# Performance work log

Measured on AMD Instinct MI355X. Metric: run time of the kernel, lower is better.

The kernel has to match this reference:

```python
import jax, jax.numpy as jnp
import numpy as np

B, S, D_MODEL, H = 2, 2048, 1024, 16
DK = D_MODEL // H
THETA = 10000.0


def setup_inputs() -> dict:
    key = jax.random.key(0)
    ks = jax.random.split(key, 5)
    scale = 0.02  # keep logits in a numerically sane range
    return {
        "x": jax.random.normal(ks[0], (B, S, D_MODEL), jnp.float32),
        "Q_weight": jax.random.normal(ks[1], (D_MODEL, D_MODEL), jnp.float32) * scale,
        "K_weight": jax.random.normal(ks[2], (D_MODEL, D_MODEL), jnp.float32) * scale,
        "V_weight": jax.random.normal(ks[3], (D_MODEL, D_MODEL), jnp.float32) * scale,
        "O_weight": jax.random.normal(ks[4], (D_MODEL, D_MODEL), jnp.float32) * scale,
        "token_positions": jnp.arange(S, dtype=jnp.int32),
    }


def _rope(x, token_positions, theta, d_k):
    # x: [..., seq, d_k]; rotate interleaved even/odd pairs
    inv_freq = 1.0 / theta ** (jnp.arange(0, d_k, 2, dtype=jnp.float32) / d_k)
    ang = token_positions.astype(jnp.float32)[:, None] * inv_freq  # [S, d_k/2]
    cos, sin = jnp.cos(ang), jnp.sin(ang)
    x0, x1 = x[..., 0::2], x[..., 1::2]
    y0 = x0 * cos - x1 * sin
    y1 = x0 * sin + x1 * cos
    return jnp.stack([y0, y1], axis=-1).reshape(x.shape)


def _mhsa(x, Qw, Kw, Vw, Ow, token_positions):
    b, s, d = x.shape
    qw = Qw.reshape(H, DK, d)
    kw = Kw.reshape(H, DK, d)
    vw = Vw.reshape(H, DK, d)
    q = jnp.einsum('hki,bsi->bhsk', qw, x)
    k = jnp.einsum('hki,bsi->bhsk', kw, x)
    v = jnp.einsum('hvi,bsi->bhsv', vw, x)
    q = _rope(q, token_positions, THETA, DK)
    k = _rope(k, token_positions, THETA, DK)
    scores = jnp.einsum('bhnd,bhmd->bhnm', q, k) / jnp.sqrt(jnp.float32(DK))
    causal = jnp.tril(jnp.ones((s, s), dtype=bool))
    scores = jnp.where(causal, scores, -jnp.inf)
    attn = jax.nn.softmax(scores, axis=-1)
    o = jnp.einsum('bhnm,bhmv->bhnv', attn, v)  # [B,H,S,DV]
    o = jnp.transpose(o, (0, 2, 1, 3)).reshape(b, s, H * DK)
    return jnp.einsum('dv,bsv->bsd', Ow, o)


def reference(x, Q_weight, K_weight, V_weight, O_weight, token_positions):
    return _mhsa(x, Q_weight, K_weight, V_weight, O_weight, token_positions)
```

## Files before the change

kernel.cpp:

```cpp
#include <hip/hip_runtime.h>

#define NB 2
#define NS 2048
#define NDM 1024
#define NH 16
#define NDK 64

typedef unsigned int u32;
typedef u32 u32x4 __attribute__((ext_vector_type(4)));
typedef float f32x4 __attribute__((ext_vector_type(4)));
typedef float f32x2 __attribute__((ext_vector_type(2)));
typedef __bf16 bf16x8 __attribute__((ext_vector_type(8)));
typedef __bf16 bf16x4 __attribute__((ext_vector_type(4)));
typedef __bf16 bf16x2 __attribute__((ext_vector_type(2)));

#define QSCALE 0.18033688011112042f
#define EXP2F(x) __builtin_amdgcn_exp2f(x)

__device__ __forceinline__ void gload_lds16(const __bf16* g, __bf16* l) {
    __builtin_amdgcn_global_load_lds(
        (const __attribute__((address_space(1))) unsigned int*)(g),
        (__attribute__((address_space(3))) unsigned int*)(l), 16, 0, 0);
}

__global__ __launch_bounds__(256) void cvt_all(const float* __restrict__ x,
                                               const float* __restrict__ qw,
                                               const float* __restrict__ kw,
                                               const float* __restrict__ vw,
                                               const float* __restrict__ ow,
                                               __bf16* __restrict__ xb,
                                               __bf16* __restrict__ wqkv,
                                               __bf16* __restrict__ owb) {
    const int i = blockIdx.x * 256 + threadIdx.x;
    const float* src;
    __bf16* dst;
    if (i < 1048576) {
        src = x + (size_t)i * 4;
        dst = xb + (size_t)i * 4;
    } else {
        const int j = i - 1048576;
        const int seg = j >> 18;
        const int off = j & 0x3FFFF;
        src = ((seg == 0) ? qw : (seg == 1) ? kw : (seg == 2) ? vw : ow) + (size_t)off * 4;
        dst = ((seg == 3) ? owb : wqkv + (size_t)seg * 1048576) + (size_t)off * 4;
    }
    f32x4 v = *(const f32x4*)src;
    bf16x4 o;
    o[0] = (__bf16)v[0]; o[1] = (__bf16)v[1]; o[2] = (__bf16)v[2]; o[3] = (__bf16)v[3];
    *(bf16x4*)dst = o;
}

__global__ __launch_bounds__(256) void rope_table(const int* __restrict__ tp,
                                                  float* __restrict__ tbl) {
    const int i = blockIdx.x * 256 + threadIdx.x;
    if (i >= NS * 32) return;
    const int s = i >> 5, jj = i & 31;
    const float pos = (float)tp[s];
    const float inv = exp2f(-0.41524101186092f * (float)jj);
    const float ang = pos * inv;
    float sn, cs;
    sincosf(ang, &sn, &cs);
    f32x2 o; o[0] = cs; o[1] = sn;
    *(f32x2*)&tbl[(size_t)i * 2] = o;
}

__global__ __launch_bounds__(512, 2) void gemm256(const __bf16* __restrict__ A,
                                                  const __bf16* __restrict__ Bt,
                                                  __bf16* __restrict__ C,
                                                  int K, int lda, int ldb, int ldc, int nbx) {
    __shared__ __bf16 As[2][256 * 64];
    __shared__ __bf16 Bs[2][256 * 64];
    const int tid = threadIdx.x;
    const int lane = tid & 63, w = tid >> 6;
    const int wm = w >> 2, wn = w & 3;
    const int l15 = lane & 15, lg = lane >> 4;
    int bid = blockIdx.x;
    const int cpx = gridDim.x >> 3;
    bid = (bid & 7) * cpx + (bid >> 3);
    const int m0 = (bid / nbx) * 256, n0 = (bid % nbx) * 256;
    const int srow = w * 8 + (lane >> 3);
    const int csw = ((lane & 7) ^ (srow & 7)) * 8;

    f32x4 acc[8][4];
    const f32x4 z = {0.f, 0.f, 0.f, 0.f};
#pragma unroll
    for (int i = 0; i < 8; ++i)
#pragma unroll
        for (int jx = 0; jx < 4; ++jx) acc[i][jx] = z;

    auto stage_pass = [&](int buf, int k0, int ps) {
        const int r = ps * 64 + srow;
        gload_lds16(&A[(size_t)(m0 + r) * lda + k0 + csw], &As[buf][(ps * 64 + w * 8) * 64]);
        gload_lds16(&Bt[(size_t)(n0 + r) * ldb + k0 + csw], &Bs[buf][(ps * 64 + w * 8) * 64]);
    };

#pragma unroll
    for (int ps = 0; ps < 4; ++ps) stage_pass(0, 0, ps);
    int cur = 0;
    for (int k0 = 0; k0 < K; k0 += 64) {
        const bool hasnext = (k0 + 64 < K);
        asm volatile("s_waitcnt vmcnt(0)" ::: "memory");
        __builtin_amdgcn_s_barrier();
        __builtin_amdgcn_sched_barrier(0);
        bf16x8 bfr[4][2];
#pragma unroll
        for (int ph = 0; ph < 4; ++ph) {
            if (ph == 0) {
#pragma unroll
                for (int n = 0; n < 4; ++n)
#pragma unroll
                    for (int kc = 0; kc < 2; ++kc) {
                        const int rb = wn * 64 + n * 16 + l15;
                        bfr[n][kc] = *(const bf16x8*)&Bs[cur][rb * 64 + ((kc * 32 + lg * 8) ^ ((rb & 7) << 3))];
                    }
            }
            bf16x8 a0[2], a1[2];
#pragma unroll
            for (int kc = 0; kc < 2; ++kc) {
                const int ra0 = wm * 128 + (2 * ph) * 16 + l15;
                const int ra1 = wm * 128 + (2 * ph + 1) * 16 + l15;
                a0[kc] = *(const bf16x8*)&As[cur][ra0 * 64 + ((kc * 32 + lg * 8) ^ ((ra0 & 7) << 3))];
                a1[kc] = *(const bf16x8*)&As[cur][ra1 * 64 + ((kc * 32 + lg * 8) ^ ((ra1 & 7) << 3))];
            }
            if (hasnext) stage_pass(cur ^ 1, k0 + 64, ph);
            __builtin_amdgcn_s_barrier();
            asm volatile("s_waitcnt lgkmcnt(0)" ::: "memory");
            __builtin_amdgcn_sched_barrier(0);
            __builtin_amdgcn_s_setprio(1);
#pragma unroll
            for (int n = 0; n < 4; ++n)
#pragma unroll
                for (int kc = 0; kc < 2; ++kc) {
                    acc[2 * ph][n]     = __builtin_amdgcn_mfma_f32_16x16x32_bf16(a0[kc], bfr[n][kc], acc[2 * ph][n], 0, 0, 0);
                    acc[2 * ph + 1][n] = __builtin_amdgcn_mfma_f32_16x16x32_bf16(a1[kc], bfr[n][kc], acc[2 * ph + 1][n], 0, 0, 0);
                }
            __builtin_amdgcn_s_setprio(0);
            __builtin_amdgcn_s_barrier();
            __builtin_amdgcn_sched_barrier(0);
        }
        cur ^= 1;
    }
#pragma unroll
    for (int mr = 0; mr < 8; ++mr)
#pragma unroll
        for (int n = 0; n < 4; ++n)
#pragma unroll
            for (int j = 0; j < 4; ++j) {
                const int row = m0 + wm * 128 + mr * 16 + lg * 4 + j;
                const int col = n0 + wn * 64 + n * 16 + l15;
                C[(size_t)row * ldc + col] = (__bf16)acc[mr][n][j];
            }
}

template <typename TOUT>
__global__ __launch_bounds__(256) void gemm_bt128(const __bf16* __restrict__ A,
                                                  const __bf16* __restrict__ Bt,
                                                  TOUT* __restrict__ C,
                                                  int K, int lda, int ldb, int ldc) {
    __shared__ __bf16 As[2][128 * 64];
    __shared__ __bf16 Bs[2][128 * 64];
    const int tid = threadIdx.x;
    const int lane = tid & 63, w = tid >> 6;
    const int wr = w >> 1, wc = w & 1;
    const int l15 = lane & 15, lg = lane >> 4;
    const int m0 = blockIdx.y * 128, n0 = blockIdx.x * 128;
    const int crow = lane >> 3;
    const int csw = ((lane & 7) ^ crow) * 8;

    f32x4 acc[4][4];
    const f32x4 z = {0.f, 0.f, 0.f, 0.f};
#pragma unroll
    for (int i = 0; i < 4; ++i)
#pragma unroll
        for (int jx = 0; jx < 4; ++jx) acc[i][jx] = z;

    auto stage = [&](int buf, int k0) {
#pragma unroll
        for (int ch = 0; ch < 4; ++ch) {
            const int cid = w * 4 + ch;
            const int ra = cid * 8 + crow;
            gload_lds16(&A[(size_t)(m0 + ra) * lda + k0 + csw], &As[buf][cid * 512]);
            gload_lds16(&Bt[(size_t)(n0 + ra) * ldb + k0 + csw], &Bs[buf][cid * 512]);
        }
    };

    stage(0, 0);
    int cur = 0;
    for (int k0 = 0; k0 < K; k0 += 64) {
        if (k0 + 64 < K) {
            stage(cur ^ 1, k0 + 64);
            asm volatile("s_waitcnt vmcnt(8)" ::: "memory");
        } else {
            asm volatile("s_waitcnt vmcnt(0)" ::: "memory");
        }
        __builtin_amdgcn_s_barrier();
        __builtin_amdgcn_sched_barrier(0);
#pragma unroll
        for (int kc = 0; kc < 2; ++kc) {
            bf16x8 af[4], bfv[4];
#pragma unroll
            for (int i = 0; i < 4; ++i) {
                const int ra = wr * 64 + i * 16 + l15;
                const int rb = wc * 64 + i * 16 + l15;
                af[i]  = *(const bf16x8*)&As[cur][ra * 64 + ((kc * 32 + lg * 8) ^ ((ra & 7) << 3))];
                bfv[i] = *(const bf16x8*)&Bs[cur][rb * 64 + ((kc * 32 + lg * 8) ^ ((rb & 7) << 3))];
            }
#pragma unroll
            for (int sm = 0; sm < 4; ++sm)
#pragma unroll
                for (int sn = 0; sn < 4; ++sn)
                    acc[sm][sn] = __builtin_amdgcn_mfma_f32_16x16x32_bf16(af[sm], bfv[sn], acc[sm][sn], 0, 0, 0);
        }
        asm volatile("s_waitcnt lgkmcnt(0)" ::: "memory");
        __builtin_amdgcn_s_barrier();
        __builtin_amdgcn_sched_barrier(0);
        cur ^= 1;
    }
#pragma unroll
    for (int sm = 0; sm < 4; ++sm)
#pragma unroll
        for (int sn = 0; sn < 4; ++sn)
#pragma unroll
            for (int j = 0; j < 4; ++j) {
                const int row = m0 + wr * 64 + sm * 16 + lg * 4 + j;
                const int col = n0 + wc * 64 + sn * 16 + l15;
                C[(size_t)row * ldc + col] = (TOUT)acc[sm][sn][j];
            }
}

__global__ __launch_bounds__(512) void rope_kernel(const __bf16* __restrict__ qkv,
                                                   const float* __restrict__ tbl,
                                                   __bf16* __restrict__ Qr,
                                                   __bf16* __restrict__ Kr) {
    const int row = blockIdx.x;
    const int s = row & (NS - 1);
    const int b = row >> 11;
    const int t = threadIdx.x;
    const int h = t >> 5, jj = t & 31;
    f32x2 cssn = *(const f32x2*)&tbl[((size_t)s * 32 + jj) * 2];
    const float cs = cssn[0], sn = cssn[1];
    const __bf16* qp = qkv + (size_t)row * 3072 + h * 64 + 2 * jj;
    bf16x2 qv = *(const bf16x2*)qp;
    bf16x2 kv = *(const bf16x2*)(qp + 1024);
    const float q0 = (float)qv[0], q1 = (float)qv[1];
    const float k0 = (float)kv[0], k1 = (float)kv[1];
    const size_t o = ((size_t)(b * NH + h) * NS + s) * 64 + 2 * jj;
    bf16x2 qo, ko;
    qo[0] = (__bf16)((q0 * cs - q1 * sn) * QSCALE);
    qo[1] = (__bf16)((q0 * sn + q1 * cs) * QSCALE);
    ko[0] = (__bf16)(k0 * cs - k1 * sn); ko[1] = (__bf16)(k0 * sn + k1 * cs);
    *(bf16x2*)&Qr[o] = qo;
    *(bf16x2*)&Kr[o] = ko;
}

__global__ __launch_bounds__(256) void vtrans(const __bf16* __restrict__ qkv,
                                              __bf16* __restrict__ Vt) {
    const int bh = blockIdx.y;
    const int s0 = blockIdx.x * 64;
    const int b = bh >> 4, h = bh & 15;
    __shared__ __bf16 tile[64][72];
    const int t = threadIdx.x;
    const int sl = t >> 3, c8 = (t & 7) * 8;
#pragma unroll
    for (int pp = 0; pp < 2; ++pp) {
        const int srow = sl + pp * 32;
        bf16x8 v = *(const bf16x8*)&qkv[(size_t)(b * NS + s0 + srow) * 3072 + 2048 + h * 64 + c8];
        *(bf16x8*)&tile[srow][c8] = v;
    }
    __syncthreads();
    const int d = t >> 2;
#pragma unroll
    for (int pp = 0; pp < 2; ++pp) {
        const int vec = (t & 3) + pp * 4;
        bf16x8 o;
#pragma unroll
        for (int i = 0; i < 8; ++i) o[i] = tile[vec * 8 + i][d];
        *(bf16x8*)&Vt[((size_t)bh * 64 + d) * NS + s0 + vec * 8] = o;
    }
}

__device__ __forceinline__ int kperm(int rt) {
    const int ct = rt >> 4, rr = rt & 15;
    return ((rr >> 2) << 3) + ((ct >> 1) << 5) + ((ct & 1) << 2) + (rr & 3);
}

__global__ __launch_bounds__(256) void attn5(const __bf16* __restrict__ Qr,
                                             const __bf16* __restrict__ Kr,
                                             const __bf16* __restrict__ Vt,
                                             __bf16* __restrict__ O) {
    const int lid = blockIdx.x;
    const int xcd = lid & 7, ix = lid >> 3;
    const int bh = xcd * 4 + (ix & 3);
    const int p  = ix >> 2;
    const int b = bh >> 4, h = bh & 15;
    const int tid = threadIdx.x;
    const int w = tid >> 6, lane = tid & 63;
    const int l15 = lane & 15, lg = lane >> 4;
    const __bf16* Qb = Qr + (size_t)bh * NS * 64;
    const __bf16* Kb = Kr + (size_t)bh * NS * 64;
    const __bf16* Vb = Vt + (size_t)bh * 64 * NS;

    __shared__ __bf16 Ks[2][64 * 64];
    __shared__ __bf16 Vs[2][64 * 64];

    const int rbv[2] = {p * 64 + w * 16, (31 - p) * 64 + w * 16};

    bf16x8 qf[2][2];
#pragma unroll
    for (int rs = 0; rs < 2; ++rs)
#pragma unroll
        for (int kc = 0; kc < 2; ++kc)
            qf[rs][kc] = *(const bf16x8*)(Qb + (size_t)(rbv[rs] + l15) * 64 + kc * 32 + lg * 8);

    f32x4 oacc[2][4];
    const f32x4 z = {0.f, 0.f, 0.f, 0.f};
#pragma unroll
    for (int rs = 0; rs < 2; ++rs)
#pragma unroll
        for (int ct = 0; ct < 4; ++ct) oacc[rs][ct] = z;
    float lsum[2] = {0.f, 0.f};

    const int crow = lane >> 3;
    const int cswz = ((lane & 7) ^ crow) * 8;

#pragma unroll
    for (int pp = 0; pp < 2; ++pp) {
        const int ch = w + pp * 4;
        const int rt = ch * 8 + crow;
        gload_lds16(Kb + (size_t)kperm(rt) * 64 + cswz, &Ks[0][ch * 512]);
        gload_lds16(Vb + (size_t)rt * NS + 0 + cswz, &Vs[0][ch * 512]);
    }
    __syncthreads();

    const int nt = 32 - p;
    for (int t = 0; t < nt; ++t) {
        const int cur = t & 1;
        const int kv0 = t << 6;
        if (t + 1 < nt) {
            const int kv1 = kv0 + 64;
#pragma unroll
            for (int pp = 0; pp < 2; ++pp) {
                const int ch = w + pp * 4;
                const int rt = ch * 8 + crow;
                gload_lds16(Kb + (size_t)(kv1 + kperm(rt)) * 64 + cswz, &Ks[cur ^ 1][ch * 512]);
                gload_lds16(Vb + (size_t)rt * NS + kv1 + cswz, &Vs[cur ^ 1][ch * 512]);
            }
        }
        bool act[2];
        act[0] = (kv0 <= rbv[0] + 15);
        act[1] = true;
        f32x4 sc[2][4];
#pragma unroll
        for (int rs = 0; rs < 2; ++rs)
            if (act[rs])
#pragma unroll
                for (int ct = 0; ct < 4; ++ct) sc[rs][ct] = z;
#pragma unroll
        for (int kc = 0; kc < 2; ++kc) {
            bf16x8 kf[4];
#pragma unroll
            for (int ct = 0; ct < 4; ++ct) {
                const int rt = ct * 16 + l15;
                kf[ct] = *(const bf16x8*)&Ks[cur][rt * 64 + ((kc * 32 + lg * 8) ^ ((rt & 7) << 3))];
            }
#pragma unroll
            for (int rs = 0; rs < 2; ++rs)
                if (act[rs])
#pragma unroll
                    for (int ct = 0; ct < 4; ++ct)
                        sc[rs][ct] = __builtin_amdgcn_mfma_f32_16x16x32_bf16(kf[ct], qf[rs][kc], sc[rs][ct], 0, 0, 0);
        }
        bf16x8 pb[2][2];
#pragma unroll
        for (int rs = 0; rs < 2; ++rs) {
            if (!act[rs]) continue;
            const int rbase = rbv[rs];
            const int qrow = rbase + l15;
            const bool needmask = (kv0 + 63 > rbase);
            if (needmask) {
#pragma unroll
                for (int ct = 0; ct < 4; ++ct)
#pragma unroll
                    for (int j = 0; j < 4; ++j) {
                        const int kvg = kv0 + ((ct >> 1) << 5) + lg * 8 + ((ct & 1) << 2) + j;
                        if (kvg > qrow) sc[rs][ct][j] = -1e30f;
                    }
            }
            float ps = 0.f;
#pragma unroll
            for (int ct = 0; ct < 4; ++ct)
#pragma unroll
                for (int j = 0; j < 4; ++j) {
                    const float e = EXP2F(sc[rs][ct][j]);
                    sc[rs][ct][j] = e;
                    ps += e;
                }
            ps += __shfl_xor(ps, 16, 64);
            ps += __shfl_xor(ps, 32, 64);
            lsum[rs] += ps;
#pragma unroll
            for (int kc = 0; kc < 2; ++kc) {
                bf16x8 pk;
                pk[0] = (__bf16)sc[rs][2 * kc][0];     pk[1] = (__bf16)sc[rs][2 * kc][1];
                pk[2] = (__bf16)sc[rs][2 * kc][2];     pk[3] = (__bf16)sc[rs][2 * kc][3];
                pk[4] = (__bf16)sc[rs][2 * kc + 1][0]; pk[5] = (__bf16)sc[rs][2 * kc + 1][1];
                pk[6] = (__bf16)sc[rs][2 * kc + 1][2]; pk[7] = (__bf16)sc[rs][2 * kc + 1][3];
                pb[rs][kc] = pk;
            }
        }
#pragma unroll
        for (int kc = 0; kc < 2; ++kc) {
            bf16x8 vf[4];
#pragma unroll
            for (int ct = 0; ct < 4; ++ct) {
                const int rt = ct * 16 + l15;
                vf[ct] = *(const bf16x8*)&Vs[cur][rt * 64 + ((kc * 32 + lg * 8) ^ ((rt & 7) << 3))];
            }
#pragma unroll
            for (int rs = 0; rs < 2; ++rs) {
                if (!act[rs]) continue;
#pragma unroll
                for (int ct = 0; ct < 4; ++ct)
                    oacc[rs][ct] = __builtin_amdgcn_mfma_f32_16x16x32_bf16(vf[ct], pb[rs][kc], oacc[rs][ct], 0, 0, 0);
            }
        }
        __syncthreads();
    }
#pragma unroll
    for (int rs = 0; rs < 2; ++rs) {
        const float rl = 1.0f / lsum[rs];
        const size_t rowoff = (size_t)(b * NS + rbv[rs] + l15) * NDM + h * 64 + lg * 4;
#pragma unroll
        for (int ct = 0; ct < 4; ++ct) {
            bf16x4 ov;
#pragma unroll
            for (int j = 0; j < 4; ++j) ov[j] = (__bf16)(oacc[rs][ct][j] * rl);
            *(bf16x4*)&O[rowoff + ct * 16] = ov;
        }
    }
}

extern "C" void kernel_launch(void* const* d_in, const int* in_sizes, int n_in,
                              void* d_out, int out_size, void* d_ws, size_t ws_size,
                              hipStream_t stream) {
    const float* x  = (const float*)d_in[0];
    const float* Qw = (const float*)d_in[1];
    const float* Kw = (const float*)d_in[2];
    const float* Vw = (const float*)d_in[3];
    const float* Ow = (const float*)d_in[4];
    const int*   tp = (const int*)d_in[5];
    float* out = (float*)d_out;

    char* ws = (char*)d_ws;
    size_t off = 0;
    auto alloc = [&](size_t bytes) -> void* {
        void* p = ws + off;
        off += (bytes + 255) & ~(size_t)255;
        return p;
    };
    __bf16* xb   = (__bf16*)alloc((size_t)4096 * 1024 * 2);
    __bf16* wqkv = (__bf16*)alloc((size_t)3072 * 1024 * 2);
    __bf16* owb  = (__bf16*)alloc((size_t)1024 * 1024 * 2);
    __bf16* qkv  = (__bf16*)alloc((size_t)4096 * 3072 * 2);
    __bf16* qr   = (__bf16*)alloc((size_t)32 * 2048 * 64 * 2);
    __bf16* kr   = (__bf16*)alloc((size_t)32 * 2048 * 64 * 2);
    __bf16* vt   = (__bf16*)alloc((size_t)32 * 64 * 2048 * 2);
    __bf16* ob   = (__bf16*)alloc((size_t)4096 * 1024 * 2);
    float*  tbl  = (float*)alloc((size_t)NS * 32 * 2 * 4);

    cvt_all<<<8192, 256, 0, stream>>>(x, Qw, Kw, Vw, Ow, xb, wqkv, owb);
    rope_table<<<(NS * 32 + 255) / 256, 256, 0, stream>>>(tp, tbl);

    gemm256<<<192, 512, 0, stream>>>(xb, wqkv, qkv, 1024, 1024, 1024, 3072, 12);
    rope_kernel<<<4096, 512, 0, stream>>>(qkv, tbl, qr, kr);
    vtrans<<<dim3(NS / 64, NB * NH), 256, 0, stream>>>(qkv, vt);
    attn5<<<dim3(512), 256, 0, stream>>>(qr, kr, vt, ob);
    gemm_bt128<float><<<dim3(1024 / 128, 4096 / 128), 256, 0, stream>>>(
        ob, owb, out, 1024, 1024, 1024, 1024);
}
```

Baseline: 119.8 us.

## Fuse V transpose into QKV GEMM epilogue and reorder attention block mapping

The QKV GEMM epilogue now writes the V third of its output straight into the transposed per-head Vt layout, using 4-wide bf16 stores along the sequence axis. This removes the separate vtrans kernel, with its extra launch and its extra read and write of V. The trade-off is that these V stores are narrower and strided rather than fully coalesced row stores. Separately, the attention kernel maps block indices to query-pair positions in an interleaved order, so heavy and light causal tiles are spread more evenly across the schedule.

New measurement: 119.1 us. No clear change (-0.6%).

```diff
diff --git a/kernel.cpp b/kernel.cpp
--- a/kernel.cpp
+++ b/kernel.cpp
@@ -67,6 +67,7 @@
 __global__ __launch_bounds__(512, 2) void gemm256(const __bf16* __restrict__ A,
                                                   const __bf16* __restrict__ Bt,
                                                   __bf16* __restrict__ C,
+                                                  __bf16* __restrict__ Vt,
                                                   int K, int lda, int ldb, int ldc, int nbx) {
     __shared__ __bf16 As[2][256 * 64];
     __shared__ __bf16 Bs[2][256 * 64];
@@ -140,16 +141,32 @@
         }
         cur ^= 1;
     }
-#pragma unroll
-    for (int mr = 0; mr < 8; ++mr)
-#pragma unroll
-        for (int n = 0; n < 4; ++n)
-#pragma unroll
-            for (int j = 0; j < 4; ++j) {
-                const int row = m0 + wm * 128 + mr * 16 + lg * 4 + j;
-                const int col = n0 + wn * 64 + n * 16 + l15;
-                C[(size_t)row * ldc + col] = (__bf16)acc[mr][n][j];
-            }
+    if (n0 < 2048) {
+#pragma unroll
+        for (int mr = 0; mr < 8; ++mr)
+#pragma unroll
+            for (int n = 0; n < 4; ++n)
+#pragma unroll
+                for (int j = 0; j < 4; ++j) {
+                    const int row = m0 + wm * 128 + mr * 16 + lg * 4 + j;
+                    const int col = n0 + wn * 64 + n * 16 + l15;
+                    C[(size_t)row * ldc + col] = (__bf16)acc[mr][n][j];
+                }
+    } else {
+#pragma unroll
+        for (int mr = 0; mr < 8; ++mr)
+#pragma unroll
+            for (int n = 0; n < 4; ++n) {
+                const int col = (n0 - 2048) + wn * 64 + n * 16 + l15;
+                const int h = col >> 6, d = col & 63;
+                const int row = m0 + wm * 128 + mr * 16 + lg * 4;
+                const int b = row >> 11, s = row & (NS - 1);
+                bf16x4 ov;
+#pragma unroll
+                for (int j = 0; j < 4; ++j) ov[j] = (__bf16)acc[mr][n][j];
+                *(bf16x4*)&Vt[((size_t)(b * NH + h) * 64 + d) * NS + s] = ov;
+            }
+    }
 }
 
 template <typename TOUT>
@@ -253,32 +270,6 @@
     *(bf16x2*)&Kr[o] = ko;
 }
 
-__global__ __launch_bounds__(256) void vtrans(const __bf16* __restrict__ qkv,
-                                              __bf16* __restrict__ Vt) {
-    const int bh = blockIdx.y;
-    const int s0 = blockIdx.x * 64;
-    const int b = bh >> 4, h = bh & 15;
-    __shared__ __bf16 tile[64][72];
-    const int t = threadIdx.x;
-    const int sl = t >> 3, c8 = (t & 7) * 8;
-#pragma unroll
-    for (int pp = 0; pp < 2; ++pp) {
-        const int srow = sl + pp * 32;
-        bf16x8 v = *(const bf16x8*)&qkv[(size_t)(b * NS + s0 + srow) * 3072 + 2048 + h * 64 + c8];
-        *(bf16x8*)&tile[srow][c8] = v;
-    }
-    __syncthreads();
-    const int d = t >> 2;
-#pragma unroll
-    for (int pp = 0; pp < 2; ++pp) {
-        const int vec = (t & 3) + pp * 4;
-        bf16x8 o;
-#pragma unroll
-        for (int i = 0; i < 8; ++i) o[i] = tile[vec * 8 + i][d];
-        *(bf16x8*)&Vt[((size_t)bh * 64 + d) * NS + s0 + vec * 8] = o;
-    }
-}
-
 __device__ __forceinline__ int kperm(int rt) {
     const int ct = rt >> 4, rr = rt & 15;
     return ((rr >> 2) << 3) + ((ct >> 1) << 5) + ((ct & 1) << 2) + (rr & 3);
@@ -289,9 +280,11 @@
                                              const __bf16* __restrict__ Vt,
                                              __bf16* __restrict__ O) {
     const int lid = blockIdx.x;
-    const int xcd = lid & 7, ix = lid >> 3;
-    const int bh = xcd * 4 + (ix & 3);
-    const int p  = ix >> 2;
+    const int xcd = lid & 7;
+    const int g = lid >> 3;
+    const int bh = xcd * 4 + (g & 3);
+    const int pr = g >> 2;
+    const int p = (pr < 8) ? (pr * 2) : (31 - 2 * pr);
     const int b = bh >> 4, h = bh & 15;
     const int tid = threadIdx.x;
     const int w = tid >> 6, lane = tid & 63;
@@ -471,9 +464,8 @@
     cvt_all<<<8192, 256, 0, stream>>>(x, Qw, Kw, Vw, Ow, xb, wqkv, owb);
     rope_table<<<(NS * 32 + 255) / 256, 256, 0, stream>>>(tp, tbl);
 
-    gemm256<<<192, 512, 0, stream>>>(xb, wqkv, qkv, 1024, 1024, 1024, 3072, 12);
+    gemm256<<<192, 512, 0, stream>>>(xb, wqkv, qkv, vt, 1024, 1024, 1024, 3072, 12);
     rope_kernel<<<4096, 512, 0, stream>>>(qkv, tbl, qr, kr);
-    vtrans<<<dim3(NS / 64, NB * NH), 256, 0, stream>>>(qkv, vt);
     attn5<<<dim3(512), 256, 0, stream>>>(qr, kr, vt, ob);
     gemm_bt128<float><<<dim3(1024 / 128, 4096 / 128), 256, 0, stream>>>(
         ob, owb, out, 1024, 1024, 1024, 1024);
```
